# Optimization experiments

Hardware: AMD Instinct MI355X
Metric: run time of the kernel (lower is better)

## Reference

```python
import jax, jax.numpy as jnp
import numpy as np

B, N, K = 2, 8192, 16
D1, D2, OUT = 128, 256, 128


def setup_inputs() -> dict:
    key = jax.random.key(0)
    ks = jax.random.split(key, 6)
    return {
        "xyz1": jax.random.normal(ks[0], (B, N, 3), dtype=jnp.float32),
        "xyz2": jax.random.normal(ks[1], (B, N, 3), dtype=jnp.float32),
        "points1": jax.random.normal(ks[2], (B, N, D1), dtype=jnp.float32),
        "points2": jax.random.normal(ks[3], (B, N, D2), dtype=jnp.float32),
        # Conv1d(k=1) == pointwise linear: weight [OUT, D1+D2], bias [OUT]
        "W": jax.random.normal(ks[4], (OUT, D1 + D2), dtype=jnp.float32) / np.sqrt(D1 + D2).astype(np.float32),
        "b": jax.random.normal(ks[5], (OUT,), dtype=jnp.float32) * 0.01,
        "nsample": K,
    }


def reference(xyz1, xyz2, points1, points2, W, b, nsample):
    Bb, Nn, _ = xyz1.shape
    # squared pairwise distances, queries=xyz2, keys=xyz1 -> [B, N, N]
    d2 = (jnp.sum(xyz2 * xyz2, -1)[:, :, None]
          + jnp.sum(xyz1 * xyz1, -1)[:, None, :]
          - 2.0 * jnp.einsum('bsc,bnc->bsn', xyz2, xyz1))
    neg_vals, idx = jax.lax.top_k(-d2, nsample)          # K nearest
    dists = -neg_vals                                     # [B, N, K] sq dists
    recip = 1.0 / (dists + 1e-8)
    weight = recip / jnp.sum(recip, axis=2, keepdims=True)  # inverse-dist weights
    # gather neighbor features from points2: [B, N, K, D2]
    g = jnp.take_along_axis(points2, idx.reshape(Bb, Nn * nsample)[:, :, None], axis=1)
    g = g.reshape(Bb, Nn, nsample, -1)
    interp = jnp.sum(g * weight[..., None], axis=2)       # [B, N, D2]
    cat = jnp.concatenate([points1, interp], axis=-1)     # [B, N, D1+D2]
    # Conv1d(kernel=1) over channel dim
    return jnp.einsum('bnc,oc->bno', cat, W) + b
```

## Files before the change

### kernel.cpp

```cpp
#include <hip/hip_runtime.h>
#include <stdint.h>

#define BQ   2
#define NQ   8192
#define D1Q  128
#define D2Q  256
#define OUTQ 128
#define CATQ 384
#define KQ   16

#define NBIN 4096
#define RED_MARGIN 1e-3f
#define LB_MARGIN  1e-2f

#define WS_WFH   0
#define WS_WFL   98304
#define WS_HIST  196608
#define WS_SPXYZ 262144
#define WS_QSXYZ 524288
#define WS_SPIDX 786432
#define WS_QSIDX 819200
#define WS_GB    851968

__device__ __forceinline__ ushort f2bf(float f) {
    uint32_t u = __float_as_uint(f);
    return (ushort)((u + 0x7FFFu + ((u >> 16) & 1u)) >> 16);
}
__device__ __forceinline__ float bf2f(ushort h) {
    return __uint_as_float((uint32_t)h << 16);
}

__device__ __forceinline__ uint32_t encf(float f) {
    uint32_t b = __float_as_uint(f);
    return b ^ (0x80000000u | (uint32_t)((int32_t)b >> 31));
}
__device__ __forceinline__ float decf(uint32_t u) {
    uint32_t bits = (u & 0x80000000u) ? (u ^ 0x80000000u) : ~u;
    return __uint_as_float(bits);
}

__device__ __forceinline__ uint32_t mbcnt64(uint64_t m) {
    return __builtin_amdgcn_mbcnt_hi((uint32_t)(m >> 32),
           __builtin_amdgcn_mbcnt_lo((uint32_t)m, 0u));
}

typedef __attribute__((ext_vector_type(8))) short short8v;
typedef __attribute__((ext_vector_type(4))) float f32x4v;

__device__ __forceinline__ int mort_bin(float x, float y, float z) {
    int bx = (int)((x + 5.0f) * 1.6f); bx = bx < 0 ? 0 : (bx > 15 ? 15 : bx);
    int by = (int)((y + 5.0f) * 1.6f); by = by < 0 ? 0 : (by > 15 ? 15 : by);
    int bz = (int)((z + 5.0f) * 1.6f); bz = bz < 0 ? 0 : (bz > 15 ? 15 : bz);
    int k = 0;
    #pragma unroll
    for (int t = 0; t < 4; ++t)
        k |= (((bx >> t) & 1) << (3 * t)) | (((by >> t) & 1) << (3 * t + 1)) |
             (((bz >> t) & 1) << (3 * t + 2));
    return k;
}

__global__ void prep_w_kernel(const float* __restrict__ W,
                              ushort* __restrict__ Wfh, ushort* __restrict__ Wfl,
                              uint32_t* __restrict__ hist,
                              uint32_t* __restrict__ gbU) {
    int flat = blockIdx.x * 256 + threadIdx.x;
    if (flat < CATQ * OUTQ) {
        int r    = flat & 7;
        int lane = (flat >> 3) & 63;
        int ctk  = flat >> 9;
        int ct   = ctk & 7;
        int kt   = ctk >> 3;
        int o = ct * 16 + (lane & 15);
        int k = kt * 32 + (lane >> 4) * 8 + r;
        float v  = W[o * CATQ + k];
        ushort h = f2bf(v);
        Wfh[flat] = h;
        Wfl[flat] = f2bf(v - bf2f(h));
    }
    if (flat < 4 * NBIN) hist[flat] = 0u;
    if (flat < 256 * 8)  gbU[flat] = ((flat & 7) >= 4) ? 0u : 0xFFFFFFFFu;
}

__global__ void hist_kernel(const float* __restrict__ xyz1,
                            const float* __restrict__ xyz2,
                            uint32_t* __restrict__ hist) {
    int i = blockIdx.x * 256 + threadIdx.x;
    if (i < BQ * NQ) {
        int batch = i >> 13;
        const float* p = xyz1 + (size_t)i * 3;
        int bin = mort_bin(p[0], p[1], p[2]);
        atomicAdd(&hist[batch * NBIN + bin], 1u);
    } else {
        int j = i - BQ * NQ;
        int batch = j >> 13;
        const float* p = xyz2 + (size_t)j * 3;
        int bin = mort_bin(p[0], p[1], p[2]);
        atomicAdd(&hist[(2 + batch) * NBIN + bin], 1u);
    }
}

__global__ void prefix_kernel(uint32_t* __restrict__ hist) {
    __shared__ uint32_t sc[1024];
    uint32_t* h = hist + (size_t)blockIdx.x * NBIN;
    int t = threadIdx.x;
    uint32_t v0 = h[4 * t], v1 = h[4 * t + 1], v2 = h[4 * t + 2], v3 = h[4 * t + 3];
    uint32_t s = v0 + v1 + v2 + v3;
    sc[t] = s;
    __syncthreads();
    for (int d = 1; d < 1024; d <<= 1) {
        uint32_t x = (t >= d) ? sc[t - d] : 0u;
        __syncthreads();
        sc[t] += x;
        __syncthreads();
    }
    uint32_t excl = sc[t] - s;
    h[4 * t]     = excl;
    h[4 * t + 1] = excl + v0;
    h[4 * t + 2] = excl + v0 + v1;
    h[4 * t + 3] = excl + v0 + v1 + v2;
}

__global__ void scatter_kernel(const float* __restrict__ xyz1,
                               const float* __restrict__ xyz2,
                               uint32_t* __restrict__ hist,
                               float4* __restrict__ sp_xyzn,
                               float4* __restrict__ qs_xyzw,
                               ushort* __restrict__ sp_idx,
                               ushort* __restrict__ qs_idx,
                               uint32_t* __restrict__ gbU) {
    int i = blockIdx.x * 256 + threadIdx.x;
    if (i < BQ * NQ) {
        int batch = i >> 13;
        const float* p = xyz1 + (size_t)i * 3;
        float x = p[0], y = p[1], z = p[2];
        int bin = mort_bin(x, y, z);
        uint32_t pos = atomicAdd(&hist[batch * NBIN + bin], 1u);
        float n;
        {
            #pragma clang fp contract(off)
            float px = x * x, py = y * y, pz = z * z;
            n = (px + py) + pz;
        }
        sp_xyzn[batch * NQ + pos] = make_float4(x, y, z, n);
        sp_idx[batch * NQ + pos]  = (ushort)(i & (NQ - 1));
        uint32_t* gw = gbU + ((size_t)batch * 128 + (pos >> 6)) * 8;
        atomicMin(&gw[0], encf(x));
        atomicMin(&gw[1], encf(y));
        atomicMin(&gw[2], encf(z));
        atomicMax(&gw[4], encf(x));
        atomicMax(&gw[5], encf(y));
        atomicMax(&gw[6], encf(z));
    } else {
        int j = i - BQ * NQ;
        int batch = j >> 13;
        const float* p = xyz2 + (size_t)j * 3;
        float x = p[0], y = p[1], z = p[2];
        int bin = mort_bin(x, y, z);
        uint32_t pos = atomicAdd(&hist[(2 + batch) * NBIN + bin], 1u);
        float s2;
        {
            #pragma clang fp contract(off)
            float px = x * x, py = y * y, pz = z * z;
            s2 = (px + py) + pz;
        }
        qs_xyzw[batch * NQ + pos] = make_float4(x, y, z, s2);
        qs_idx[batch * NQ + pos]  = (ushort)(j & (NQ - 1));
    }
}

__device__ __forceinline__ float npy_d2(float4 pt, float qx, float qy, float qz,
                                        float s2) {
    #pragma clang fp contract(off)
    float d0  = pt.x * qx;
    float dot = fmaf(pt.y, qy, d0);
    dot       = fmaf(pt.z, qz, dot);
    float tt  = s2 + pt.w;
    return tt - 2.0f * dot;
}

__device__ __forceinline__ float red_r(float4 pt, float qx, float qy, float qz) {
    float dot = fmaf(pt.z, qz, fmaf(pt.y, qy, pt.x * qx));
    return fmaf(-2.0f, dot, pt.w);
}

__device__ __forceinline__ uint64_t sort64(uint64_t x, int lane) {
    #pragma unroll
    for (int k = 2; k <= 64; k <<= 1) {
        #pragma unroll
        for (int j = k >> 1; j > 0; j >>= 1) {
            uint64_t p = __shfl_xor((unsigned long long)x, j, 64);
            bool keep_min = (((lane & j) == 0) == ((lane & k) == 0));
            bool pless    = p < x;
            x = (pless == keep_min) ? p : x;
        }
    }
    return x;
}

__global__ __launch_bounds__(256, 4) void fused_kernel(
        const float4* __restrict__ sp_xyzn, const ushort* __restrict__ sp_idx,
        const float4* __restrict__ qs_xyzw, const ushort* __restrict__ qs_idx,
        const float* __restrict__ points1, const float* __restrict__ points2,
        const ushort* __restrict__ Wfh, const ushort* __restrict__ Wfl,
        const float* __restrict__ bias, const uint32_t* __restrict__ gbU,
        float* __restrict__ out) {
    __shared__ __align__(16) char smem[26368];
    uint64_t* wball = (uint64_t*)smem;
    ushort*   cat_h = (ushort*)smem;
    ushort*   cat_l = (ushort*)(smem + 12544);
    ushort*   slist = (ushort*)(smem + 25088);
    ushort*   qsl   = (ushort*)(smem + 26112);

    const int tid   = threadIdx.x;
    const int lane  = tid & 63;
    const int w     = tid >> 6;
    const int blk   = blockIdx.x;
    const int b     = blk >> 9;
    const int qslot = (blk & 511) * 16;

    if (tid < 16) qsl[tid] = qs_idx[b * NQ + qslot + tid];

    float qx[4], qy[4], qz[4], s2[4];
    int   oqi[4];
    #pragma unroll
    for (int j = 0; j < 4; ++j) {
        float4 q = qs_xyzw[(size_t)b * NQ + qslot + w * 4 + j];
        qx[j] = q.x; qy[j] = q.y; qz[j] = q.z; s2[j] = q.w;
        oqi[j] = (int)qs_idx[b * NQ + qslot + w * 4 + j];
    }

    const float4* spb = sp_xyzn + (size_t)b * NQ;
    const ushort* spi = sp_idx  + (size_t)b * NQ;

    int wstart = qslot + 8 - 512;
    if (wstart < 0) wstart = 0;
    if (wstart > NQ - 1024) wstart = NQ - 1024;
    wstart &= ~63;
    const float4* win = spb + wstart;

    float mn[4];
    #pragma unroll
    for (int j = 0; j < 4; ++j) mn[j] = __uint_as_float(0x7F800000u);

    #pragma unroll 4
    for (int s = 0; s < 16; ++s) {
        float4 pt = win[s * 64 + lane];
        #pragma unroll
        for (int j = 0; j < 4; ++j)
            mn[j] = fminf(mn[j], red_r(pt, qx[j], qy[j], qz[j]));
    }

    float that[4];
    #pragma unroll
    for (int j = 0; j < 4; ++j) {
        float x = mn[j];
        #pragma unroll
        for (int k = 2; k <= 64; k <<= 1) {
            #pragma unroll
            for (int jj = k >> 1; jj > 0; jj >>= 1) {
                float px = __shfl_xor(x, jj, 64);
                bool keep_min = (((lane & jj) == 0) == ((lane & k) == 0));
                float mnv = fminf(x, px), mxv = fmaxf(x, px);
                x = keep_min ? mnv : mxv;
            }
        }
        that[j] = s2[j] + __shfl(x, 15, 64) + RED_MARGIN;
    }

    ushort* sl = slist + w * 128;
    int scnt_w = 0;
    {
        float qlx = fminf(fminf(qx[0], qx[1]), fminf(qx[2], qx[3]));
        float qly = fminf(fminf(qy[0], qy[1]), fminf(qy[2], qy[3]));
        float qlz = fminf(fminf(qz[0], qz[1]), fminf(qz[2], qz[3]));
        float qhx = fmaxf(fmaxf(qx[0], qx[1]), fmaxf(qx[2], qx[3]));
        float qhy = fmaxf(fmaxf(qy[0], qy[1]), fmaxf(qy[2], qy[3]));
        float qhz = fmaxf(fmaxf(qz[0], qz[1]), fmaxf(qz[2], qz[3]));
        float tmax = fmaxf(fmaxf(that[0], that[1]), fmaxf(that[2], that[3]))
                   + LB_MARGIN;
        #pragma unroll
        for (int h = 0; h < 2; ++h) {
            int g = h * 64 + lane;
            const uint32_t* gw = gbU + ((size_t)b * 128 + g) * 8;
            float glx = decf(gw[0]), gly = decf(gw[1]), glz = decf(gw[2]);
            float ghx = decf(gw[4]), ghy = decf(gw[5]), ghz = decf(gw[6]);
            float dx = fmaxf(fmaxf(qlx - ghx, glx - qhx), 0.f);
            float dy = fmaxf(fmaxf(qly - ghy, gly - qhy), 0.f);
            float dz = fmaxf(fmaxf(qlz - ghz, glz - qhz), 0.f);
            float lb = dx * dx;
            lb = fmaf(dy, dy, lb);
            lb = fmaf(dz, dz, lb);
            bool sv = (lb <= tmax);
            uint64_t m = __ballot((int)sv);
            if (sv) sl[scnt_w + mbcnt64(m)] = (ushort)g;
            scnt_w += (int)__popcll(m);
        }
    }

    uint32_t cnt[4] = {0u, 0u, 0u, 0u};
    for (int i = 0; i < scnt_w; ++i) {
        const int g = (int)sl[i];
        float4   pt   = spb[g * 64 + lane];
        uint32_t pidx = (uint32_t)spi[g * 64 + lane];
        #pragma unroll
        for (int j = 0; j < 4; ++j) {
            float d2 = npy_d2(pt, qx[j], qy[j], qz[j], s2[j]);
            bool  v  = (d2 <= that[j]);
            uint64_t mask = __ballot((int)v);
            if (mask != 0ull) {
                if (v) {
                    uint32_t pos    = cnt[j] + mbcnt64(mask);
                    uint32_t bits   = __float_as_uint(d2);
                    uint32_t mapped = bits ^ (0x80000000u |
                                      (uint32_t)((int32_t)bits >> 31));
                    if (pos < 128u)
                        wball[(w * 4 + j) * 128 + pos] =
                            ((uint64_t)mapped << 32) | (uint64_t)pidx;
                }
                cnt[j] += (uint32_t)__popcll(mask);
            }
        }
    }

    int   myidxA[4];
    float mywgtA[4];
    #pragma unroll
    for (int j = 0; j < 4; ++j) {
        const uint64_t* wb = wball + (size_t)(w * 4 + j) * 128;
        const uint32_t c = cnt[j];
        uint64_t mykey;
        if (c <= 64u) {
            uint64_t k0 = (lane < (int)c) ? wb[lane] : ~0ull;
            mykey = sort64(k0, lane);
        } else {
            uint32_t cc = c > 128u ? 128u : c;
            uint64_t k0 = wb[lane];
            uint64_t k1 = (lane + 64 < (int)cc) ? wb[lane + 64] : ~0ull;
            k0 = sort64(k0, lane);
            k1 = sort64(k1, lane);
            uint64_t t1 = __shfl((unsigned long long)k1, lane & 15, 64);
            uint64_t km = (lane < 16) ? k0 : ((lane < 32) ? t1 : ~0ull);
            mykey = sort64(km, lane);
        }
        uint32_t mhi   = (uint32_t)(mykey >> 32);
        uint32_t rbits = (mhi & 0x80000000u) ? (mhi ^ 0x80000000u) : ~mhi;
        float    d2w   = __uint_as_float(rbits);
        myidxA[j] = (int)(uint32_t)(mykey & 0xFFFFFFFFull);
        float recip = (lane < KQ) ? (1.0f / (d2w + 1e-8f)) : 0.0f;
        float tot = recip;
        #pragma unroll
        for (int sh = 1; sh < 16; sh <<= 1) tot += __shfl_xor(tot, sh, 64);
        mywgtA[j] = recip / tot;
    }

    __syncthreads();

    const float* p2b = points2 + (size_t)b * NQ * D2Q;
    #pragma unroll
    for (int j = 0; j < 4; ++j) {
        const int qi = w * 4 + j;
        if (lane < 32) {
            float4 p = ((const float4*)(points1 +
                        (size_t)(b * NQ + oqi[j]) * D1Q))[lane];
            ushort4 hv, lv;
            hv.x = f2bf(p.x); lv.x = f2bf(p.x - bf2f(hv.x));
            hv.y = f2bf(p.y); lv.y = f2bf(p.y - bf2f(hv.y));
            hv.z = f2bf(p.z); lv.z = f2bf(p.z - bf2f(hv.z));
            hv.w = f2bf(p.w); lv.w = f2bf(p.w - bf2f(hv.w));
            *(ushort4*)&cat_h[qi * 392 + lane * 4] = hv;
            *(ushort4*)&cat_l[qi * 392 + lane * 4] = lv;
        }
        float4 acc = make_float4(0.f, 0.f, 0.f, 0.f);
        #pragma unroll
        for (int k = 0; k < KQ; ++k) {
            int   kk = __builtin_amdgcn_readlane(myidxA[j], k);
            float wk = __uint_as_float((uint32_t)__builtin_amdgcn_readlane(
                           (int)__float_as_uint(mywgtA[j]), k));
            float4 row = ((const float4*)(p2b + (size_t)kk * D2Q))[lane];
            acc.x = fmaf(wk, row.x, acc.x);
            acc.y = fmaf(wk, row.y, acc.y);
            acc.z = fmaf(wk, row.z, acc.z);
            acc.w = fmaf(wk, row.w, acc.w);
        }
        {
            ushort4 hv, lv;
            hv.x = f2bf(acc.x); lv.x = f2bf(acc.x - bf2f(hv.x));
            hv.y = f2bf(acc.y); lv.y = f2bf(acc.y - bf2f(hv.y));
            hv.z = f2bf(acc.z); lv.z = f2bf(acc.z - bf2f(hv.z));
            hv.w = f2bf(acc.w); lv.w = f2bf(acc.w - bf2f(hv.w));
            *(ushort4*)&cat_h[qi * 392 + D1Q + lane * 4] = hv;
            *(ushort4*)&cat_l[qi * 392 + D1Q + lane * 4] = lv;
        }
    }
    __syncthreads();

    {
        const int arow = lane & 15;
        const int koff = (lane >> 4) * 8;
        const int ct0  = w * 2;
        f32x4v acc0 = {0.f, 0.f, 0.f, 0.f};
        f32x4v acc1 = {0.f, 0.f, 0.f, 0.f};
        #pragma unroll 4
        for (int kt = 0; kt < 12; ++kt) {
            short8v ah = *(const short8v*)&cat_h[arow * 392 + kt * 32 + koff];
            short8v al = *(const short8v*)&cat_l[arow * 392 + kt * 32 + koff];
            const ushort* bhp = Wfh + ((size_t)(kt * 8 + ct0) * 64 + lane) * 8;
            const ushort* blp = Wfl + ((size_t)(kt * 8 + ct0) * 64 + lane) * 8;
            short8v bh0 = *(const short8v*)bhp;
            short8v bl0 = *(const short8v*)blp;
            short8v bh1 = *(const short8v*)(bhp + 512);
            short8v bl1 = *(const short8v*)(blp + 512);
            acc0 = __builtin_amdgcn_mfma_f32_16x16x32_bf16(ah, bh0, acc0, 0, 0, 0);
            acc0 = __builtin_amdgcn_mfma_f32_16x16x32_bf16(al, bh0, acc0, 0, 0, 0);
            acc0 = __builtin_amdgcn_mfma_f32_16x16x32_bf16(ah, bl0, acc0, 0, 0, 0);
            acc1 = __builtin_amdgcn_mfma_f32_16x16x32_bf16(ah, bh1, acc1, 0, 0, 0);
            acc1 = __builtin_amdgcn_mfma_f32_16x16x32_bf16(al, bh1, acc1, 0, 0, 0);
            acc1 = __builtin_amdgcn_mfma_f32_16x16x32_bf16(ah, bl1, acc1, 0, 0, 0);
        }
        const int col0   = ct0 * 16 + (lane & 15);
        const int r0slot = (lane >> 4) * 4;
        const float bv0 = bias[col0];
        const float bv1 = bias[col0 + 16];
        #pragma unroll
        for (int r = 0; r < 4; ++r) {
            int oq = (int)qsl[r0slot + r];
            size_t rowoff = (size_t)(b * NQ + oq) * OUTQ;
            out[rowoff + col0]      = acc0[r] + bv0;
            out[rowoff + col0 + 16] = acc1[r] + bv1;
        }
    }
}

extern "C" void kernel_launch(void* const* d_in, const int* in_sizes, int n_in,
                              void* d_out, int out_size, void* d_ws, size_t ws_size,
                              hipStream_t stream) {
    const float* xyz1    = (const float*)d_in[0];
    const float* xyz2    = (const float*)d_in[1];
    const float* points1 = (const float*)d_in[2];
    const float* points2 = (const float*)d_in[3];
    const float* W       = (const float*)d_in[4];
    const float* bias    = (const float*)d_in[5];

    char* ws = (char*)d_ws;
    ushort*   Wfh     = (ushort*)(ws + WS_WFH);
    ushort*   Wfl     = (ushort*)(ws + WS_WFL);
    uint32_t* hist    = (uint32_t*)(ws + WS_HIST);
    float4*   sp_xyzn = (float4*)(ws + WS_SPXYZ);
    float4*   qs_xyzw = (float4*)(ws + WS_QSXYZ);
    ushort*   sp_idx  = (ushort*)(ws + WS_SPIDX);
    ushort*   qs_idx  = (ushort*)(ws + WS_QSIDX);
    uint32_t* gbU     = (uint32_t*)(ws + WS_GB);

    prep_w_kernel<<<192, 256, 0, stream>>>(W, Wfh, Wfl, hist, gbU);
    hist_kernel<<<128, 256, 0, stream>>>(xyz1, xyz2, hist);
    prefix_kernel<<<4, 1024, 0, stream>>>(hist);
    scatter_kernel<<<128, 256, 0, stream>>>(xyz1, xyz2, hist,
                                            sp_xyzn, qs_xyzw, sp_idx, qs_idx, gbU);
    fused_kernel<<<(BQ * NQ) / 16, 256, 0, stream>>>(
        sp_xyzn, sp_idx, qs_xyzw, qs_idx, points1, points2,
        Wfh, Wfl, bias, gbU, (float*)d_out);
}
```

Measured before the change: 179.2 us.

## Fuse preprocessing kernels into one block-local sort kernel and prefetch neighbor groups

Four preprocessing launches (weight prep, histogram, prefix scan, scatter) are merged into one kernel. Each of four blocks sorts one batch/cloud entirely in shared memory, and the remaining blocks convert the weights. Group bounding boxes are now built with shared-memory atomics and stored as decoded float4, so the fused kernel does not decode them. The fused kernel also remaps block order across batches and raises an unroll factor. Its candidate scan software-prefetches points two groups ahead. The aim is to cut launch overhead and global atomics. The trade-off is that the sort now runs on only four blocks, so it is serialized on a few CUs.

```diff
diff --git a/kernel.cpp b/kernel.cpp
--- a/kernel.cpp
+++ b/kernel.cpp
@@ -15,12 +15,12 @@
 
 #define WS_WFH   0
 #define WS_WFL   98304
-#define WS_HIST  196608
 #define WS_SPXYZ 262144
 #define WS_QSXYZ 524288
 #define WS_SPIDX 786432
 #define WS_QSIDX 819200
-#define WS_GB    851968
+#define WS_GBLO  851968
+#define WS_GBHI  856064
 
 __device__ __forceinline__ ushort f2bf(float f) {
     uint32_t u = __float_as_uint(f);
@@ -59,112 +59,112 @@
     return k;
 }
 
-__global__ void prep_w_kernel(const float* __restrict__ W,
-                              ushort* __restrict__ Wfh, ushort* __restrict__ Wfl,
-                              uint32_t* __restrict__ hist,
-                              uint32_t* __restrict__ gbU) {
-    int flat = blockIdx.x * 256 + threadIdx.x;
-    if (flat < CATQ * OUTQ) {
-        int r    = flat & 7;
-        int lane = (flat >> 3) & 63;
-        int ctk  = flat >> 9;
-        int ct   = ctk & 7;
-        int kt   = ctk >> 3;
-        int o = ct * 16 + (lane & 15);
-        int k = kt * 32 + (lane >> 4) * 8 + r;
-        float v  = W[o * CATQ + k];
-        ushort h = f2bf(v);
-        Wfh[flat] = h;
-        Wfl[flat] = f2bf(v - bf2f(h));
-    }
-    if (flat < 4 * NBIN) hist[flat] = 0u;
-    if (flat < 256 * 8)  gbU[flat] = ((flat & 7) >= 4) ? 0u : 0xFFFFFFFFu;
-}
-
-__global__ void hist_kernel(const float* __restrict__ xyz1,
-                            const float* __restrict__ xyz2,
-                            uint32_t* __restrict__ hist) {
-    int i = blockIdx.x * 256 + threadIdx.x;
-    if (i < BQ * NQ) {
-        int batch = i >> 13;
-        const float* p = xyz1 + (size_t)i * 3;
-        int bin = mort_bin(p[0], p[1], p[2]);
-        atomicAdd(&hist[batch * NBIN + bin], 1u);
-    } else {
-        int j = i - BQ * NQ;
-        int batch = j >> 13;
-        const float* p = xyz2 + (size_t)j * 3;
-        int bin = mort_bin(p[0], p[1], p[2]);
-        atomicAdd(&hist[(2 + batch) * NBIN + bin], 1u);
-    }
-}
-
-__global__ void prefix_kernel(uint32_t* __restrict__ hist) {
+__global__ __launch_bounds__(1024) void prep_all_kernel(
+        const float* __restrict__ W,
+        ushort* __restrict__ Wfh, ushort* __restrict__ Wfl,
+        const float* __restrict__ xyz1, const float* __restrict__ xyz2,
+        float4* __restrict__ sp_xyzn, float4* __restrict__ qs_xyzw,
+        ushort* __restrict__ sp_idx, ushort* __restrict__ qs_idx,
+        float4* __restrict__ gblo, float4* __restrict__ gbhi) {
+    __shared__ uint32_t hist[NBIN];
     __shared__ uint32_t sc[1024];
-    uint32_t* h = hist + (size_t)blockIdx.x * NBIN;
-    int t = threadIdx.x;
-    uint32_t v0 = h[4 * t], v1 = h[4 * t + 1], v2 = h[4 * t + 2], v3 = h[4 * t + 3];
+    __shared__ uint32_t ab[128 * 8];
+
+    const int bid = blockIdx.x;
+    const int tid = threadIdx.x;
+
+    if (bid >= 4) {
+        int flat = (bid - 4) * 1024 + tid;
+        if (flat < CATQ * OUTQ) {
+            int r    = flat & 7;
+            int lane = (flat >> 3) & 63;
+            int ctk  = flat >> 9;
+            int ct   = ctk & 7;
+            int kt   = ctk >> 3;
+            int o = ct * 16 + (lane & 15);
+            int k = kt * 32 + (lane >> 4) * 8 + r;
+            float v  = W[o * CATQ + k];
+            ushort h = f2bf(v);
+            Wfh[flat] = h;
+            Wfl[flat] = f2bf(v - bf2f(h));
+        }
+        return;
+    }
+
+    const int  batch = bid & 1;
+    const bool isPts = bid < 2;
+    const float* src = (isPts ? xyz1 : xyz2) + (size_t)batch * NQ * 3;
+
+    #pragma unroll
+    for (int i = tid; i < NBIN; i += 1024) hist[i] = 0u;
+    if (isPts) ab[tid] = ((tid & 7) >= 4) ? 0u : 0xFFFFFFFFu;
+    __syncthreads();
+
+    float x[8], y[8], z[8];
+    int   bin[8];
+    #pragma unroll
+    for (int e = 0; e < 8; ++e) {
+        int idx = e * 1024 + tid;
+        const float* p = src + (size_t)idx * 3;
+        x[e] = p[0]; y[e] = p[1]; z[e] = p[2];
+        bin[e] = mort_bin(x[e], y[e], z[e]);
+        atomicAdd(&hist[bin[e]], 1u);
+    }
+    __syncthreads();
+
+    uint32_t v0 = hist[4 * tid], v1 = hist[4 * tid + 1],
+             v2 = hist[4 * tid + 2], v3 = hist[4 * tid + 3];
     uint32_t s = v0 + v1 + v2 + v3;
-    sc[t] = s;
+    sc[tid] = s;
     __syncthreads();
     for (int d = 1; d < 1024; d <<= 1) {
-        uint32_t x = (t >= d) ? sc[t - d] : 0u;
+        uint32_t xx = (tid >= d) ? sc[tid - d] : 0u;
         __syncthreads();
-        sc[t] += x;
+        sc[tid] += xx;
         __syncthreads();
     }
-    uint32_t excl = sc[t] - s;
-    h[4 * t]     = excl;
-    h[4 * t + 1] = excl + v0;
-    h[4 * t + 2] = excl + v0 + v1;
-    h[4 * t + 3] = excl + v0 + v1 + v2;
-}
-
-__global__ void scatter_kernel(const float* __restrict__ xyz1,
-                               const float* __restrict__ xyz2,
-                               uint32_t* __restrict__ hist,
-                               float4* __restrict__ sp_xyzn,
-                               float4* __restrict__ qs_xyzw,
-                               ushort* __restrict__ sp_idx,
-                               ushort* __restrict__ qs_idx,
-                               uint32_t* __restrict__ gbU) {
-    int i = blockIdx.x * 256 + threadIdx.x;
-    if (i < BQ * NQ) {
-        int batch = i >> 13;
-        const float* p = xyz1 + (size_t)i * 3;
-        float x = p[0], y = p[1], z = p[2];
-        int bin = mort_bin(x, y, z);
-        uint32_t pos = atomicAdd(&hist[batch * NBIN + bin], 1u);
+    uint32_t excl = sc[tid] - s;
+    hist[4 * tid]     = excl;
+    hist[4 * tid + 1] = excl + v0;
+    hist[4 * tid + 2] = excl + v0 + v1;
+    hist[4 * tid + 3] = excl + v0 + v1 + v2;
+    __syncthreads();
+
+    #pragma unroll
+    for (int e = 0; e < 8; ++e) {
+        int idx = e * 1024 + tid;
+        uint32_t pos = atomicAdd(&hist[bin[e]], 1u);
         float n;
         {
             #pragma clang fp contract(off)
-            float px = x * x, py = y * y, pz = z * z;
+            float px = x[e] * x[e], py = y[e] * y[e], pz = z[e] * z[e];
             n = (px + py) + pz;
         }
-        sp_xyzn[batch * NQ + pos] = make_float4(x, y, z, n);
-        sp_idx[batch * NQ + pos]  = (ushort)(i & (NQ - 1));
-        uint32_t* gw = gbU + ((size_t)batch * 128 + (pos >> 6)) * 8;
-        atomicMin(&gw[0], encf(x));
-        atomicMin(&gw[1], encf(y));
-        atomicMin(&gw[2], encf(z));
-        atomicMax(&gw[4], encf(x));
-        atomicMax(&gw[5], encf(y));
-        atomicMax(&gw[6], encf(z));
-    } else {
-        int j = i - BQ * NQ;
-        int batch = j >> 13;
-        const float* p = xyz2 + (size_t)j * 3;
-        float x = p[0], y = p[1], z = p[2];
-        int bin = mort_bin(x, y, z);
-        uint32_t pos = atomicAdd(&hist[(2 + batch) * NBIN + bin], 1u);
-        float s2;
-        {
-            #pragma clang fp contract(off)
-            float px = x * x, py = y * y, pz = z * z;
-            s2 = (px + py) + pz;
-        }
-        qs_xyzw[batch * NQ + pos] = make_float4(x, y, z, s2);
-        qs_idx[batch * NQ + pos]  = (ushort)(j & (NQ - 1));
+        if (isPts) {
+            sp_xyzn[batch * NQ + pos] = make_float4(x[e], y[e], z[e], n);
+            sp_idx[batch * NQ + pos]  = (ushort)idx;
+            uint32_t* gw = ab + ((pos >> 6) << 3);
+            atomicMin(&gw[0], encf(x[e]));
+            atomicMin(&gw[1], encf(y[e]));
+            atomicMin(&gw[2], encf(z[e]));
+            atomicMax(&gw[4], encf(x[e]));
+            atomicMax(&gw[5], encf(y[e]));
+            atomicMax(&gw[6], encf(z[e]));
+        } else {
+            qs_xyzw[batch * NQ + pos] = make_float4(x[e], y[e], z[e], n);
+            qs_idx[batch * NQ + pos]  = (ushort)idx;
+        }
+    }
+    if (isPts) {
+        __syncthreads();
+        if (tid < 128) {
+            gblo[batch * 128 + tid] = make_float4(
+                decf(ab[tid * 8 + 0]), decf(ab[tid * 8 + 1]),
+                decf(ab[tid * 8 + 2]), 0.f);
+            gbhi[batch * 128 + tid] = make_float4(
+                decf(ab[tid * 8 + 4]), decf(ab[tid * 8 + 5]),
+                decf(ab[tid * 8 + 6]), 0.f);
+        }
     }
 }
 
@@ -202,7 +202,8 @@
         const float4* __restrict__ qs_xyzw, const ushort* __restrict__ qs_idx,
         const float* __restrict__ points1, const float* __restrict__ points2,
         const ushort* __restrict__ Wfh, const ushort* __restrict__ Wfl,
-        const float* __restrict__ bias, const uint32_t* __restrict__ gbU,
+        const float* __restrict__ bias,
+        const float4* __restrict__ gblo, const float4* __restrict__ gbhi,
         float* __restrict__ out) {
     __shared__ __align__(16) char smem[26368];
     uint64_t* wball = (uint64_t*)smem;
@@ -214,7 +215,7 @@
     const int tid   = threadIdx.x;
     const int lane  = tid & 63;
     const int w     = tid >> 6;
-    const int blk   = blockIdx.x;
+    const int blk   = (blockIdx.x & 7) * 128 + (blockIdx.x >> 3);
     const int b     = blk >> 9;
     const int qslot = (blk & 511) * 16;
 
@@ -242,7 +243,7 @@
     #pragma unroll
     for (int j = 0; j < 4; ++j) mn[j] = __uint_as_float(0x7F800000u);
 
-    #pragma unroll 4
+    #pragma unroll 8
     for (int s = 0; s < 16; ++s) {
         float4 pt = win[s * 64 + lane];
         #pragma unroll
@@ -281,12 +282,11 @@
         #pragma unroll
         for (int h = 0; h < 2; ++h) {
             int g = h * 64 + lane;
-            const uint32_t* gw = gbU + ((size_t)b * 128 + g) * 8;
-            float glx = decf(gw[0]), gly = decf(gw[1]), glz = decf(gw[2]);
-            float ghx = decf(gw[4]), ghy = decf(gw[5]), ghz = decf(gw[6]);
-            float dx = fmaxf(fmaxf(qlx - ghx, glx - qhx), 0.f);
-            float dy = fmaxf(fmaxf(qly - ghy, gly - qhy), 0.f);
-            float dz = fmaxf(fmaxf(qlz - ghz, glz - qhz), 0.f);
+            float4 gl = gblo[b * 128 + g];
+            float4 gh = gbhi[b * 128 + g];
+            float dx = fmaxf(fmaxf(qlx - gh.x, gl.x - qhx), 0.f);
+            float dy = fmaxf(fmaxf(qly - gh.y, gl.y - qhy), 0.f);
+            float dz = fmaxf(fmaxf(qlz - gh.z, gl.z - qhz), 0.f);
             float lb = dx * dx;
             lb = fmaf(dy, dy, lb);
             lb = fmaf(dz, dz, lb);
@@ -298,26 +298,43 @@
     }
 
     uint32_t cnt[4] = {0u, 0u, 0u, 0u};
-    for (int i = 0; i < scnt_w; ++i) {
-        const int g = (int)sl[i];
-        float4   pt   = spb[g * 64 + lane];
-        uint32_t pidx = (uint32_t)spi[g * 64 + lane];
-        #pragma unroll
-        for (int j = 0; j < 4; ++j) {
-            float d2 = npy_d2(pt, qx[j], qy[j], qz[j], s2[j]);
-            bool  v  = (d2 <= that[j]);
-            uint64_t mask = __ballot((int)v);
-            if (mask != 0ull) {
-                if (v) {
-                    uint32_t pos    = cnt[j] + mbcnt64(mask);
-                    uint32_t bits   = __float_as_uint(d2);
-                    uint32_t mapped = bits ^ (0x80000000u |
-                                      (uint32_t)((int32_t)bits >> 31));
-                    if (pos < 128u)
-                        wball[(w * 4 + j) * 128 + pos] =
-                            ((uint64_t)mapped << 32) | (uint64_t)pidx;
+    {
+        float4 ptA = make_float4(0.f, 0.f, 0.f, 0.f), ptB = ptA;
+        uint32_t pA = 0u, pB = 0u;
+        if (scnt_w > 0) {
+            int g = (int)sl[0];
+            ptA = spb[g * 64 + lane]; pA = (uint32_t)spi[g * 64 + lane];
+        }
+        if (scnt_w > 1) {
+            int g = (int)sl[1];
+            ptB = spb[g * 64 + lane]; pB = (uint32_t)spi[g * 64 + lane];
+        }
+        for (int i = 0; i < scnt_w; ++i) {
+            float4   pt   = ptA;
+            uint32_t pidx = pA;
+            ptA = ptB; pA = pB;
+            if (i + 2 < scnt_w) {
+                int g = (int)sl[i + 2];
+                ptB = spb[g * 64 + lane];
+                pB  = (uint32_t)spi[g * 64 + lane];
+            }
+            #pragma unroll
+            for (int j = 0; j < 4; ++j) {
+                float d2 = npy_d2(pt, qx[j], qy[j], qz[j], s2[j]);
+                bool  v  = (d2 <= that[j]);
+                uint64_t mask = __ballot((int)v);
+                if (mask != 0ull) {
+                    if (v) {
+                        uint32_t pos    = cnt[j] + mbcnt64(mask);
+                        uint32_t bits   = __float_as_uint(d2);
+                        uint32_t mapped = bits ^ (0x80000000u |
+                                          (uint32_t)((int32_t)bits >> 31));
+                        if (pos < 128u)
+                            wball[(w * 4 + j) * 128 + pos] =
+                                ((uint64_t)mapped << 32) | (uint64_t)pidx;
+                    }
+                    cnt[j] += (uint32_t)__popcll(mask);
                 }
-                cnt[j] += (uint32_t)__popcll(mask);
             }
         }
     }
@@ -444,19 +461,17 @@
     char* ws = (char*)d_ws;
     ushort*   Wfh     = (ushort*)(ws + WS_WFH);
     ushort*   Wfl     = (ushort*)(ws + WS_WFL);
-    uint32_t* hist    = (uint32_t*)(ws + WS_HIST);
     float4*   sp_xyzn = (float4*)(ws + WS_SPXYZ);
     float4*   qs_xyzw = (float4*)(ws + WS_QSXYZ);
     ushort*   sp_idx  = (ushort*)(ws + WS_SPIDX);
     ushort*   qs_idx  = (ushort*)(ws + WS_QSIDX);
-    uint32_t* gbU     = (uint32_t*)(ws + WS_GB);
-
-    prep_w_kernel<<<192, 256, 0, stream>>>(W, Wfh, Wfl, hist, gbU);
-    hist_kernel<<<128, 256, 0, stream>>>(xyz1, xyz2, hist);
-    prefix_kernel<<<4, 1024, 0, stream>>>(hist);
-    scatter_kernel<<<128, 256, 0, stream>>>(xyz1, xyz2, hist,
-                                            sp_xyzn, qs_xyzw, sp_idx, qs_idx, gbU);
+    float4*   gblo    = (float4*)(ws + WS_GBLO);
+    float4*   gbhi    = (float4*)(ws + WS_GBHI);
+
+    prep_all_kernel<<<52, 1024, 0, stream>>>(W, Wfh, Wfl, xyz1, xyz2,
+                                             sp_xyzn, qs_xyzw, sp_idx, qs_idx,
+                                             gblo, gbhi);
     fused_kernel<<<(BQ * NQ) / 16, 256, 0, stream>>>(
         sp_xyzn, sp_idx, qs_xyzw, qs_idx, points1, points2,
-        Wfh, Wfl, bias, gbU, (float*)d_out);
-}
+        Wfh, Wfl, bias, gblo, gbhi, (float*)d_out);
+}
```

After: 152.7 us. 14.8% less time.
